# Kernel tuning notes

Measured on AMD Instinct MI355X. Metric: run time of the kernel, lower is better.

## Reference

```python
import jax, jax.numpy as jnp
import numpy as np

D_MODEL = 1024
N_HEADS = 16
HEAD_DIM = D_MODEL // N_HEADS
B, S = 4, 2048


def setup_inputs() -> dict:
    key = jax.random.key(0)
    ks = jax.random.split(key, 11)
    scale = 1.0 / np.sqrt(D_MODEL)
    inp = {
        "query": jax.random.normal(ks[0], (B, S, D_MODEL), jnp.float32),
        "key": jax.random.normal(ks[1], (B, S, D_MODEL), jnp.float32),
        "value": jax.random.normal(ks[2], (B, S, D_MODEL), jnp.float32),
        "Wq": jax.random.normal(ks[3], (D_MODEL, D_MODEL), jnp.float32) * scale,
        "bq": jnp.zeros((D_MODEL,), jnp.float32),
        "Wk": jax.random.normal(ks[4], (D_MODEL, D_MODEL), jnp.float32) * scale,
        "bk": jnp.zeros((D_MODEL,), jnp.float32),
        "Wv": jax.random.normal(ks[5], (D_MODEL, D_MODEL), jnp.float32) * scale,
        "bv": jnp.zeros((D_MODEL,), jnp.float32),
        "Wo": jax.random.normal(ks[6], (D_MODEL, D_MODEL), jnp.float32) * scale,
        "bo": jnp.zeros((D_MODEL,), jnp.float32),
    }
    return inp


def _split_heads(x):
    b, s, _ = x.shape
    return x.reshape(b, s, N_HEADS, HEAD_DIM).transpose(0, 2, 1, 3)  # b h s d


def reference(query, key, value, Wq, bq, Wk, bk, Wv, bv, Wo, bo):
    Q = _split_heads(query @ Wq.T + bq)
    K = _split_heads(key @ Wk.T + bk)
    V = _split_heads(value @ Wv.T + bv)
    scale = 1.0 / jnp.sqrt(jnp.float32(HEAD_DIM))
    energy = jnp.einsum("bhqd,bhkd->bhqk", Q, K) * scale  # full N x N scores
    attn = jax.nn.softmax(energy, axis=-1)
    x = jnp.einsum("bhqk,bhkd->bhqd", attn, V)
    x = x.transpose(0, 2, 1, 3).reshape(query.shape[0], -1, D_MODEL)
    return x @ Wo.T + bo
```

## Files before the change

kernel.cpp:

```cpp
#include <hip/hip_runtime.h>
#include <cstdint>
#include <cstddef>


typedef unsigned short u16;
typedef unsigned u32;
typedef short short8 __attribute__((ext_vector_type(8)));
typedef __bf16 bf16x8 __attribute__((ext_vector_type(8)));
typedef float f32x4 __attribute__((ext_vector_type(4)));
typedef float f32x16 __attribute__((ext_vector_type(16)));
typedef unsigned short u16x4 __attribute__((ext_vector_type(4)));
typedef unsigned u32x2 __attribute__((ext_vector_type(2)));
typedef unsigned u32x4 __attribute__((ext_vector_type(4)));
typedef int iv2 __attribute__((ext_vector_type(2)));

__device__ __forceinline__ u16 f2bf(float f) {
  unsigned u = __builtin_bit_cast(unsigned, f);
  u += 0x7fffu + ((u >> 16) & 1u);
  return (u16)(u >> 16);
}
__device__ __forceinline__ bf16x8 bc8(short8 v) { return __builtin_bit_cast(bf16x8, v); }
__device__ __forceinline__ u32 pk_bf16(float a, float b) {
  u32 r;
  asm("v_cvt_pk_bf16_f32 %0, %1, %2" : "=v"(r) : "v"(a), "v"(b));
  return r;
}
__device__ __forceinline__ void gload16(const u16* g, u16* l) {
  __builtin_amdgcn_global_load_lds((const __attribute__((address_space(1))) void*)g,
                                   (__attribute__((address_space(3))) void*)l, 16, 0, 0);
}

__global__ __launch_bounds__(256) void cvt_all(const float* __restrict__ q,
                                               const float* __restrict__ k,
                                               const float* __restrict__ v,
                                               const float* __restrict__ wq,
                                               const float* __restrict__ wk,
                                               const float* __restrict__ wv,
                                               const float* __restrict__ wo,
                                               u16* __restrict__ xq, u16* __restrict__ xk,
                                               u16* __restrict__ xv, u16* __restrict__ wqb,
                                               u16* __restrict__ wkb, u16* __restrict__ wvb,
                                               u16* __restrict__ wob) {
  const size_t i4 = (size_t)blockIdx.x * 256 + threadIdx.x;
  const size_t A4 = 1ull << 21, W4 = 1ull << 18;
  const float* s;
  u16* d;
  size_t off;
  if (i4 < 3 * A4) {
    const int r = (int)(i4 >> 21);
    off = i4 & (A4 - 1);
    s = r == 0 ? q : (r == 1 ? k : v);
    d = r == 0 ? xq : (r == 1 ? xk : xv);
  } else {
    const size_t t = i4 - 3 * A4;
    const int r = (int)(t >> 18);
    off = t & (W4 - 1);
    s = r == 0 ? wq : (r == 1 ? wk : (r == 2 ? wv : wo));
    d = r == 0 ? wqb : (r == 1 ? wkb : (r == 2 ? wvb : wob));
  }
  const f32x4 a = ((const f32x4*)s)[off];
  u32x2 o = {pk_bf16(a[0], a[1]), pk_bf16(a[2], a[3])};
  ((u32x2*)d)[off] = o;
}

__device__ __forceinline__ bf16x8 ldf(const u16* buf, int row, int g) {
  return bc8(*(const short8*)(buf + row * 32 + g * 8));
}

__device__ __forceinline__ void gemm_core(u16* lds, const u16* __restrict__ A,
                                          const u16* __restrict__ Bw,
                                          const float* __restrict__ bias,
                                          void* __restrict__ C, int mode, float oscale) {
  const int t = threadIdx.x;
  const int w = t >> 6, l = t & 63, g = l >> 4, m = l & 15;
  const int wr = w >> 1, wc = w & 1;
  const int m0 = blockIdx.x * 128, n0 = blockIdx.y * 256;
  const u16* gA = A + (size_t)m0 * 1024;
  const u16* gB = Bw + (size_t)n0 * 1024;

  f32x4 acc[4][8];
  const f32x4 z = {0.f, 0.f, 0.f, 0.f};
#pragma unroll
  for (int i = 0; i < 4; ++i)
#pragma unroll
    for (int j = 0; j < 8; ++j) acc[i][j] = z;

#pragma unroll
  for (int tt = 0; tt < 2; ++tt) {
    u16* sA = lds + tt * 12288;
    u16* sB = sA + 4096;
    const int ko = tt * 32;
#pragma unroll
    for (int r = 0; r < 2; ++r) {
      const int c = r * 256 + t;
      gload16(gA + (size_t)(c >> 2) * 1024 + (c & 3) * 8 + ko, sA + c * 8);
    }
#pragma unroll
    for (int r = 0; r < 4; ++r) {
      const int c = r * 256 + t;
      gload16(gB + (size_t)(c >> 2) * 1024 + (c & 3) * 8 + ko, sB + c * 8);
    }
  }
  asm volatile("s_waitcnt vmcnt(6)" ::: "memory");
  __builtin_amdgcn_s_barrier();

  bf16x8 af[4], bfr[8];
  int cb = 0;
  for (int tt = 0; tt < 32; ++tt) {
    u16* bA = lds + cb * 12288;
    u16* bB = bA + 4096;
    const int sbi = (cb == 0) ? 2 : cb - 1;
    u16* sA = lds + sbi * 12288;
    u16* sB = sA + 4096;
    const int ko = (tt + 2) * 32;
    const bool st = tt < 30;

    af[0] = ldf(bA, wr * 64 + m, g);
    af[1] = ldf(bA, wr * 64 + 16 + m, g);
#pragma unroll
    for (int j = 0; j < 4; ++j) bfr[j] = ldf(bB, wc * 128 + j * 16 + m, g);
    if (st) {
#pragma unroll
      for (int r = 0; r < 2; ++r) {
        const int c = r * 256 + t;
        gload16(gA + (size_t)(c >> 2) * 1024 + (c & 3) * 8 + ko, sA + c * 8);
      }
    }
    __builtin_amdgcn_s_barrier();
    __builtin_amdgcn_s_setprio(1);
#pragma unroll
    for (int i = 0; i < 2; ++i)
#pragma unroll
      for (int j = 0; j < 4; ++j)
        acc[i][j] = __builtin_amdgcn_mfma_f32_16x16x32_bf16(af[i], bfr[j], acc[i][j], 0, 0, 0);
    __builtin_amdgcn_s_setprio(0);
    __builtin_amdgcn_s_barrier();

#pragma unroll
    for (int j = 4; j < 8; ++j) bfr[j] = ldf(bB, wc * 128 + j * 16 + m, g);
    if (st) {
#pragma unroll
      for (int r = 0; r < 2; ++r) {
        const int c = r * 256 + t;
        gload16(gB + (size_t)(c >> 2) * 1024 + (c & 3) * 8 + ko, sB + c * 8);
      }
    }
    __builtin_amdgcn_s_barrier();
    __builtin_amdgcn_s_setprio(1);
#pragma unroll
    for (int i = 0; i < 2; ++i)
#pragma unroll
      for (int j = 4; j < 8; ++j)
        acc[i][j] = __builtin_amdgcn_mfma_f32_16x16x32_bf16(af[i], bfr[j], acc[i][j], 0, 0, 0);
    __builtin_amdgcn_s_setprio(0);
    __builtin_amdgcn_s_barrier();

    af[2] = ldf(bA, wr * 64 + 32 + m, g);
    af[3] = ldf(bA, wr * 64 + 48 + m, g);
    if (st) {
#pragma unroll
      for (int r = 2; r < 4; ++r) {
        const int c = r * 256 + t;
        gload16(gB + (size_t)(c >> 2) * 1024 + (c & 3) * 8 + ko, sB + c * 8);
      }
    }
    __builtin_amdgcn_s_barrier();
    __builtin_amdgcn_s_setprio(1);
#pragma unroll
    for (int i = 2; i < 4; ++i)
#pragma unroll
      for (int j = 0; j < 4; ++j)
        acc[i][j] = __builtin_amdgcn_mfma_f32_16x16x32_bf16(af[i], bfr[j], acc[i][j], 0, 0, 0);
    __builtin_amdgcn_s_setprio(0);
    __builtin_amdgcn_s_barrier();

    __builtin_amdgcn_s_setprio(1);
#pragma unroll
    for (int i = 2; i < 4; ++i)
#pragma unroll
      for (int j = 4; j < 8; ++j)
        acc[i][j] = __builtin_amdgcn_mfma_f32_16x16x32_bf16(af[i], bfr[j], acc[i][j], 0, 0, 0);
    __builtin_amdgcn_s_setprio(0);
    if (tt < 30)
      asm volatile("s_waitcnt vmcnt(6)" ::: "memory");
    else
      asm volatile("s_waitcnt vmcnt(0)" ::: "memory");
    __builtin_amdgcn_s_barrier();
    cb = (cb == 2) ? 0 : cb + 1;
  }

  float bv[8];
#pragma unroll
  for (int j = 0; j < 8; ++j) bv[j] = bias[n0 + wc * 128 + j * 16 + m];

  if (mode == 2) {
#pragma unroll
    for (int i = 0; i < 4; ++i)
#pragma unroll
      for (int j = 0; j < 8; ++j) {
        const int row0 = m0 + wr * 64 + i * 16 + g * 4;
        const int col = n0 + wc * 128 + j * 16 + m;
        u16x4 o;
#pragma unroll
        for (int r = 0; r < 4; ++r) o[r] = f2bf((acc[i][j][r] + bv[j]) * oscale);
        *(u16x4*)((u16*)C + ((size_t)(row0 >> 11) * 1024 + col) * 2048 + (row0 & 2047)) = o;
      }
  } else {
#pragma unroll
    for (int i = 0; i < 4; ++i) {
#pragma unroll
      for (int r = 0; r < 4; ++r) {
        const int row = m0 + wr * 64 + i * 16 + g * 4 + r;
#pragma unroll
        for (int j = 0; j < 8; ++j) {
          const int col = n0 + wc * 128 + j * 16 + m;
          const float v = (acc[i][j][r] + bv[j]) * oscale;
          if (mode == 0)
            ((float*)C)[(size_t)row * 1024 + col] = v;
          else
            ((u16*)C)[(size_t)row * 1024 + col] = f2bf(v);
        }
      }
    }
  }
}

__global__ __launch_bounds__(256, 2) void qkv_gemm(const u16* __restrict__ xq,
                                                   const u16* __restrict__ xk,
                                                   const u16* __restrict__ xv,
                                                   const u16* __restrict__ wqb,
                                                   const u16* __restrict__ wkb,
                                                   const u16* __restrict__ wvb,
                                                   const float* __restrict__ bq,
                                                   const float* __restrict__ bk,
                                                   const float* __restrict__ bv,
                                                   u16* __restrict__ Qp, u16* __restrict__ Kp,
                                                   u16* __restrict__ Vt, float SC) {
  __shared__ alignas(16) u16 lds[36864];
  const int z = blockIdx.z;
  const u16* A = z == 0 ? xq : (z == 1 ? xk : xv);
  const u16* W = z == 0 ? wqb : (z == 1 ? wkb : wvb);
  const float* bi = z == 0 ? bq : (z == 1 ? bk : bv);
  void* C = z == 0 ? (void*)Qp : (z == 1 ? (void*)Kp : (void*)Vt);
  gemm_core(lds, A, W, bi, C, z == 2 ? 2 : 1, z == 0 ? SC : 1.f);
}

__global__ __launch_bounds__(256, 2) void o_gemm(const u16* __restrict__ Xa,
                                                 const u16* __restrict__ wob,
                                                 const float* __restrict__ bo,
                                                 float* __restrict__ out) {
  __shared__ alignas(16) u16 lds[36864];
  gemm_core(lds, Xa, wob, bo, out, 0, 1.f);
}

__global__ __launch_bounds__(256, 4) void attn_fwd(const u16* __restrict__ Q,
                                                   const u16* __restrict__ Kp,
                                                   const u16* __restrict__ Vt,
                                                   u16* __restrict__ Xa) {
  __shared__ alignas(16) u16 kl[2][64][72];
  __shared__ alignas(16) u16 vl[2][64][72];
  const int tid = threadIdx.x;
  const int l = tid & 63, w = tid >> 6;
  const int q32 = l & 31, hi = l >> 5;
  const int lin = blockIdx.x + 16 * blockIdx.y;
  const int xp = lin >> 6, yp = lin & 63;
  const int b = yp >> 4, h = yp & 15;
  const int q0 = xp * 128 + w * 32;

  bf16x8 qf[4];
  const size_t qrow = (size_t)b * 2048 + q0 + q32;
#pragma unroll
  for (int ds = 0; ds < 4; ++ds)
    qf[ds] = bc8(*(const short8*)(Q + qrow * 1024 + h * 64 + ds * 16 + hi * 8));

  f32x16 of[2] = {{}, {}};
  float l0 = 0.f, l1 = 0.f, l2 = 0.f, l3 = 0.f;

  const int sr = tid >> 3;
  const int sc8 = (tid & 7) * 8;
  const u16* Kb = Kp + (size_t)b * 2048 * 1024 + h * 64;
  const u16* Vb = Vt + (size_t)yp * 64 * 2048;

  short8 rk[2], rv[2];
#pragma unroll
  for (int it = 0; it < 2; ++it) {
    const int r = sr + it * 32;
    rk[it] = *(const short8*)(Kb + (size_t)r * 1024 + sc8);
    rv[it] = *(const short8*)(Vb + (size_t)r * 2048 + sc8);
    *(short8*)(&kl[0][r][sc8]) = rk[it];
    *(short8*)(&vl[0][r][sc8]) = rv[it];
  }
#pragma unroll
  for (int it = 0; it < 2; ++it) {
    const int r = sr + it * 32;
    rk[it] = *(const short8*)(Kb + (size_t)(64 + r) * 1024 + sc8);
    rv[it] = *(const short8*)(Vb + (size_t)r * 2048 + 64 + sc8);
  }
  asm volatile("s_waitcnt lgkmcnt(0)\n\ts_barrier" ::: "memory");

  for (int kt = 0; kt < 32; ++kt) {
    const int cur = kt & 1;

    f32x16 st2[2];
    __builtin_amdgcn_s_setprio(1);
#pragma unroll
    for (int kt2 = 0; kt2 < 2; ++kt2) {
      f32x16 st = {};
#pragma unroll
      for (int ds = 0; ds < 4; ++ds) {
        const bf16x8 kf = bc8(*(const short8*)(&kl[cur][kt2 * 32 + q32][ds * 16 + hi * 8]));
        st = __builtin_amdgcn_mfma_f32_32x32x16_bf16(kf, qf[ds], st, 0, 0, 0);
      }
      st2[kt2] = st;
    }
    __builtin_amdgcn_s_setprio(0);

    if (kt + 1 < 32) {
#pragma unroll
      for (int it = 0; it < 2; ++it) {
        const int r = sr + it * 32;
        *(short8*)(&kl[cur ^ 1][r][sc8]) = rk[it];
        *(short8*)(&vl[cur ^ 1][r][sc8]) = rv[it];
      }
    }
    if (kt + 2 < 32) {
#pragma unroll
      for (int it = 0; it < 2; ++it) {
        const int r = sr + it * 32;
        rk[it] = *(const short8*)(Kb + (size_t)((kt + 2) * 64 + r) * 1024 + sc8);
        rv[it] = *(const short8*)(Vb + (size_t)r * 2048 + (kt + 2) * 64 + sc8);
      }
    }

#pragma unroll
    for (int kt2 = 0; kt2 < 2; ++kt2) {
      float p[16];
#pragma unroll
      for (int r = 0; r < 16; ++r) p[r] = __builtin_amdgcn_exp2f(st2[kt2][r]);
      l0 += (p[0] + p[1]) + (p[2] + p[3]);
      l1 += (p[4] + p[5]) + (p[6] + p[7]);
      l2 += (p[8] + p[9]) + (p[10] + p[11]);
      l3 += (p[12] + p[13]) + (p[14] + p[15]);
#pragma unroll
      for (int s = 0; s < 2; ++s) {
        int X0 = (int)pk_bf16(p[8 * s + 0], p[8 * s + 1]);
        int X1 = (int)pk_bf16(p[8 * s + 2], p[8 * s + 3]);
        int Y0 = (int)pk_bf16(p[8 * s + 4], p[8 * s + 5]);
        int Y1 = (int)pk_bf16(p[8 * s + 6], p[8 * s + 7]);
        iv2 r0 = __builtin_amdgcn_permlane32_swap(X0, Y0, false, false);
        iv2 r1 = __builtin_amdgcn_permlane32_swap(X1, Y1, false, false);
        u32x4 bw = {(u32)r0[0], (u32)r1[0], (u32)r0[1], (u32)r1[1]};
        const bf16x8 pb = __builtin_bit_cast(bf16x8, bw);
        const int ks = kt2 * 2 + s;
        __builtin_amdgcn_s_setprio(1);
#pragma unroll
        for (int dt = 0; dt < 2; ++dt) {
          const bf16x8 vf = bc8(*(const short8*)(&vl[cur][dt * 32 + q32][ks * 16 + hi * 8]));
          of[dt] = __builtin_amdgcn_mfma_f32_32x32x16_bf16(vf, pb, of[dt], 0, 0, 0);
        }
        __builtin_amdgcn_s_setprio(0);
      }
    }
    asm volatile("s_waitcnt lgkmcnt(0)\n\ts_barrier" ::: "memory");
  }

  float lo = (l0 + l1) + (l2 + l3);
  lo += __shfl_xor(lo, 32, 64);
  const float inv = 1.0f / lo;

#pragma unroll
  for (int dt = 0; dt < 2; ++dt)
#pragma unroll
    for (int rg = 0; rg < 4; ++rg) {
      u32x2 o2;
      o2[0] = pk_bf16(of[dt][4 * rg + 0] * inv, of[dt][4 * rg + 1] * inv);
      o2[1] = pk_bf16(of[dt][4 * rg + 2] * inv, of[dt][4 * rg + 3] * inv);
      *(u32x2*)(Xa + qrow * 1024 + h * 64 + dt * 32 + rg * 8 + hi * 4) = o2;
    }
}

extern "C" void kernel_launch(void* const* d_in, const int* in_sizes, int n_in,
                              void* d_out, int out_size, void* d_ws, size_t ws_size,
                              hipStream_t stream) {
  const float* q  = (const float*)d_in[0];
  const float* k  = (const float*)d_in[1];
  const float* v  = (const float*)d_in[2];
  const float* Wq = (const float*)d_in[3];
  const float* bq = (const float*)d_in[4];
  const float* Wk = (const float*)d_in[5];
  const float* bk = (const float*)d_in[6];
  const float* Wv = (const float*)d_in[7];
  const float* bv = (const float*)d_in[8];
  const float* Wo = (const float*)d_in[9];
  const float* bo = (const float*)d_in[10];

  char* ws = (char*)d_ws;
  const size_t MB = 1024ull * 1024ull;
  u16* wqb = (u16*)(ws + 0 * MB);
  u16* wkb = (u16*)(ws + 2 * MB);
  u16* wvb = (u16*)(ws + 4 * MB);
  u16* wob = (u16*)(ws + 6 * MB);
  u16* xq  = (u16*)(ws + 8 * MB);
  u16* xk  = (u16*)(ws + 24 * MB);
  u16* xv  = (u16*)(ws + 40 * MB);
  u16* Qp  = (u16*)(ws + 56 * MB);
  u16* Kp  = (u16*)(ws + 72 * MB);
  u16* Vt  = (u16*)(ws + 88 * MB);
  u16* Xa  = xq;

  cvt_all<<<28672, 256, 0, stream>>>(q, k, v, Wq, Wk, Wv, Wo,
                                     xq, xk, xv, wqb, wkb, wvb, wob);

  const float SC = 0.125f * 1.44269504f;
  qkv_gemm<<<dim3(64, 4, 3), 256, 0, stream>>>(xq, xk, xv, wqb, wkb, wvb,
                                               bq, bk, bv, Qp, Kp, Vt, SC);

  attn_fwd<<<dim3(16, 64), 256, 0, stream>>>(Qp, Kp, Vt, Xa);

  o_gemm<<<dim3(64, 4), 256, 0, stream>>>(Xa, wob, bo, (float*)d_out);
}
```

Baseline: 200.9 us.

## Process two 32-row query groups per wave in attention to reuse K/V fragments

Each wave now computes 64 query rows as two 32-row groups that share the same K and V LDS fragments. The grid is halved, so each block covers 256 queries. This cuts K/V global loads and LDS reads per query and raises the ratio of MFMA work to memory traffic. In exchange, register pressure roughly doubles, launch bounds drop to 2 blocks per SM, and there are fewer blocks to hide latency.

```diff
diff --git a/kernel.cpp b/kernel.cpp
--- a/kernel.cpp
+++ b/kernel.cpp
@@ -253,7 +253,7 @@
   gemm_core(lds, Xa, wob, bo, out, 0, 1.f);
 }
 
-__global__ __launch_bounds__(256, 4) void attn_fwd(const u16* __restrict__ Q,
+__global__ __launch_bounds__(256, 2) void attn_fwd(const u16* __restrict__ Q,
                                                    const u16* __restrict__ Kp,
                                                    const u16* __restrict__ Vt,
                                                    u16* __restrict__ Xa) {
@@ -262,19 +262,21 @@
   const int tid = threadIdx.x;
   const int l = tid & 63, w = tid >> 6;
   const int q32 = l & 31, hi = l >> 5;
-  const int lin = blockIdx.x + 16 * blockIdx.y;
+  const int lin = blockIdx.x + 8 * blockIdx.y;
   const int xp = lin >> 6, yp = lin & 63;
   const int b = yp >> 4, h = yp & 15;
-  const int q0 = xp * 128 + w * 32;
-
-  bf16x8 qf[4];
+  const int q0 = xp * 256 + w * 64;
+
+  bf16x8 qf[2][4];
   const size_t qrow = (size_t)b * 2048 + q0 + q32;
 #pragma unroll
-  for (int ds = 0; ds < 4; ++ds)
-    qf[ds] = bc8(*(const short8*)(Q + qrow * 1024 + h * 64 + ds * 16 + hi * 8));
-
-  f32x16 of[2] = {{}, {}};
-  float l0 = 0.f, l1 = 0.f, l2 = 0.f, l3 = 0.f;
+  for (int qg = 0; qg < 2; ++qg)
+#pragma unroll
+    for (int ds = 0; ds < 4; ++ds)
+      qf[qg][ds] = bc8(*(const short8*)(Q + (qrow + qg * 32) * 1024 + h * 64 + ds * 16 + hi * 8));
+
+  f32x16 of[2][2] = {{{}, {}}, {{}, {}}};
+  float ls[2][4] = {{0.f, 0.f, 0.f, 0.f}, {0.f, 0.f, 0.f, 0.f}};
 
   const int sr = tid >> 3;
   const int sc8 = (tid & 7) * 8;
@@ -301,62 +303,76 @@
   for (int kt = 0; kt < 32; ++kt) {
     const int cur = kt & 1;
 
-    f32x16 st2[2];
-    __builtin_amdgcn_s_setprio(1);
 #pragma unroll
     for (int kt2 = 0; kt2 < 2; ++kt2) {
-      f32x16 st = {};
-#pragma unroll
-      for (int ds = 0; ds < 4; ++ds) {
-        const bf16x8 kf = bc8(*(const short8*)(&kl[cur][kt2 * 32 + q32][ds * 16 + hi * 8]));
-        st = __builtin_amdgcn_mfma_f32_32x32x16_bf16(kf, qf[ds], st, 0, 0, 0);
-      }
-      st2[kt2] = st;
-    }
-    __builtin_amdgcn_s_setprio(0);
-
-    if (kt + 1 < 32) {
-#pragma unroll
-      for (int it = 0; it < 2; ++it) {
-        const int r = sr + it * 32;
-        *(short8*)(&kl[cur ^ 1][r][sc8]) = rk[it];
-        *(short8*)(&vl[cur ^ 1][r][sc8]) = rv[it];
-      }
-    }
-    if (kt + 2 < 32) {
-#pragma unroll
-      for (int it = 0; it < 2; ++it) {
-        const int r = sr + it * 32;
-        rk[it] = *(const short8*)(Kb + (size_t)((kt + 2) * 64 + r) * 1024 + sc8);
-        rv[it] = *(const short8*)(Vb + (size_t)r * 2048 + (kt + 2) * 64 + sc8);
-      }
-    }
-
-#pragma unroll
-    for (int kt2 = 0; kt2 < 2; ++kt2) {
-      float p[16];
-#pragma unroll
-      for (int r = 0; r < 16; ++r) p[r] = __builtin_amdgcn_exp2f(st2[kt2][r]);
-      l0 += (p[0] + p[1]) + (p[2] + p[3]);
-      l1 += (p[4] + p[5]) + (p[6] + p[7]);
-      l2 += (p[8] + p[9]) + (p[10] + p[11]);
-      l3 += (p[12] + p[13]) + (p[14] + p[15]);
+      bf16x8 kf[4];
+#pragma unroll
+      for (int ds = 0; ds < 4; ++ds)
+        kf[ds] = bc8(*(const short8*)(&kl[cur][kt2 * 32 + q32][ds * 16 + hi * 8]));
+      f32x16 st[2];
+      __builtin_amdgcn_s_setprio(1);
+#pragma unroll
+      for (int qg = 0; qg < 2; ++qg) {
+        f32x16 s = {};
+#pragma unroll
+        for (int ds = 0; ds < 4; ++ds)
+          s = __builtin_amdgcn_mfma_f32_32x32x16_bf16(kf[ds], qf[qg][ds], s, 0, 0, 0);
+        st[qg] = s;
+      }
+      __builtin_amdgcn_s_setprio(0);
+
+      if (kt2 == 0) {
+        if (kt + 1 < 32) {
+#pragma unroll
+          for (int it = 0; it < 2; ++it) {
+            const int r = sr + it * 32;
+            *(short8*)(&kl[cur ^ 1][r][sc8]) = rk[it];
+            *(short8*)(&vl[cur ^ 1][r][sc8]) = rv[it];
+          }
+        }
+        if (kt + 2 < 32) {
+#pragma unroll
+          for (int it = 0; it < 2; ++it) {
+            const int r = sr + it * 32;
+            rk[it] = *(const short8*)(Kb + (size_t)((kt + 2) * 64 + r) * 1024 + sc8);
+            rv[it] = *(const short8*)(Vb + (size_t)r * 2048 + (kt + 2) * 64 + sc8);
+          }
+        }
+      }
+
+      bf16x8 pbf[2][2];
+#pragma unroll
+      for (int qg = 0; qg < 2; ++qg) {
+        float p[16];
+#pragma unroll
+        for (int r = 0; r < 16; ++r) p[r] = __builtin_amdgcn_exp2f(st[qg][r]);
+        ls[qg][0] += (p[0] + p[1]) + (p[2] + p[3]);
+        ls[qg][1] += (p[4] + p[5]) + (p[6] + p[7]);
+        ls[qg][2] += (p[8] + p[9]) + (p[10] + p[11]);
+        ls[qg][3] += (p[12] + p[13]) + (p[14] + p[15]);
+#pragma unroll
+        for (int s = 0; s < 2; ++s) {
+          int X0 = (int)pk_bf16(p[8 * s + 0], p[8 * s + 1]);
+          int X1 = (int)pk_bf16(p[8 * s + 2], p[8 * s + 3]);
+          int Y0 = (int)pk_bf16(p[8 * s + 4], p[8 * s + 5]);
+          int Y1 = (int)pk_bf16(p[8 * s + 6], p[8 * s + 7]);
+          iv2 r0 = __builtin_amdgcn_permlane32_swap(X0, Y0, false, false);
+          iv2 r1 = __builtin_amdgcn_permlane32_swap(X1, Y1, false, false);
+          u32x4 bw = {(u32)r0[0], (u32)r1[0], (u32)r0[1], (u32)r1[1]};
+          pbf[qg][s] = __builtin_bit_cast(bf16x8, bw);
+        }
+      }
+
 #pragma unroll
       for (int s = 0; s < 2; ++s) {
-        int X0 = (int)pk_bf16(p[8 * s + 0], p[8 * s + 1]);
-        int X1 = (int)pk_bf16(p[8 * s + 2], p[8 * s + 3]);
-        int Y0 = (int)pk_bf16(p[8 * s + 4], p[8 * s + 5]);
-        int Y1 = (int)pk_bf16(p[8 * s + 6], p[8 * s + 7]);
-        iv2 r0 = __builtin_amdgcn_permlane32_swap(X0, Y0, false, false);
-        iv2 r1 = __builtin_amdgcn_permlane32_swap(X1, Y1, false, false);
-        u32x4 bw = {(u32)r0[0], (u32)r1[0], (u32)r0[1], (u32)r1[1]};
-        const bf16x8 pb = __builtin_bit_cast(bf16x8, bw);
         const int ks = kt2 * 2 + s;
         __builtin_amdgcn_s_setprio(1);
 #pragma unroll
         for (int dt = 0; dt < 2; ++dt) {
           const bf16x8 vf = bc8(*(const short8*)(&vl[cur][dt * 32 + q32][ks * 16 + hi * 8]));
-          of[dt] = __builtin_amdgcn_mfma_f32_32x32x16_bf16(vf, pb, of[dt], 0, 0, 0);
+#pragma unroll
+          for (int qg = 0; qg < 2; ++qg)
+            of[qg][dt] = __builtin_amdgcn_mfma_f32_32x32x16_bf16(vf, pbf[qg][s], of[qg][dt], 0, 0, 0);
         }
         __builtin_amdgcn_s_setprio(0);
       }
@@ -364,19 +380,22 @@
     asm volatile("s_waitcnt lgkmcnt(0)\n\ts_barrier" ::: "memory");
   }
 
-  float lo = (l0 + l1) + (l2 + l3);
-  lo += __shfl_xor(lo, 32, 64);
-  const float inv = 1.0f / lo;
-
-#pragma unroll
-  for (int dt = 0; dt < 2; ++dt)
-#pragma unroll
-    for (int rg = 0; rg < 4; ++rg) {
-      u32x2 o2;
-      o2[0] = pk_bf16(of[dt][4 * rg + 0] * inv, of[dt][4 * rg + 1] * inv);
-      o2[1] = pk_bf16(of[dt][4 * rg + 2] * inv, of[dt][4 * rg + 3] * inv);
-      *(u32x2*)(Xa + qrow * 1024 + h * 64 + dt * 32 + rg * 8 + hi * 4) = o2;
-    }
+#pragma unroll
+  for (int qg = 0; qg < 2; ++qg) {
+    float lo = (ls[qg][0] + ls[qg][1]) + (ls[qg][2] + ls[qg][3]);
+    lo += __shfl_xor(lo, 32, 64);
+    const float inv = 1.0f / lo;
+    const size_t qr = qrow + qg * 32;
+#pragma unroll
+    for (int dt = 0; dt < 2; ++dt)
+#pragma unroll
+      for (int rg = 0; rg < 4; ++rg) {
+        u32x2 o2;
+        o2[0] = pk_bf16(of[qg][dt][4 * rg + 0] * inv, of[qg][dt][4 * rg + 1] * inv);
+        o2[1] = pk_bf16(of[qg][dt][4 * rg + 2] * inv, of[qg][dt][4 * rg + 3] * inv);
+        *(u32x2*)(Xa + qr * 1024 + h * 64 + dt * 32 + rg * 8 + hi * 4) = o2;
+      }
+  }
 }
 
 extern "C" void kernel_launch(void* const* d_in, const int* in_sizes, int n_in,
@@ -415,7 +434,7 @@
   qkv_gemm<<<dim3(64, 4, 3), 256, 0, stream>>>(xq, xk, xv, wqb, wkb, wvb,
                                                bq, bk, bv, Qp, Kp, Vt, SC);
 
-  attn_fwd<<<dim3(16, 64), 256, 0, stream>>>(Qp, Kp, Vt, Xa);
+  attn_fwd<<<dim3(8, 64), 256, 0, stream>>>(Qp, Kp, Vt, Xa);
 
   o_gemm<<<dim3(64, 4), 256, 0, stream>>>(Xa, wob, bo, (float*)d_out);
 }
```

After: 195.0 us. 2.9% less time.
